# Performance work log

Measured on AMD Instinct MI355X. Metric: run time of the kernel, lower is better.

The kernel has to match this reference:

```python
import jax, jax.numpy as jnp
import numpy as np

B, S, H, V, T = 32, 128, 256, 32000, 100


def setup_inputs() -> dict:
    key = jax.random.key(0)
    ks = jax.random.split(key, 16)
    s = 1.0 / np.sqrt(H)

    def u(k, shape):
        return jax.random.uniform(k, shape, jnp.float32, -s, s)

    return dict(
        enc_outputs=jax.random.normal(ks[0], (B, S, H), jnp.float32),
        enc_hidden=jax.random.normal(ks[1], (1, B, H), jnp.float32),
        target_tensor=jax.random.randint(ks[2], (B, T), 0, V),
        embedding=u(ks[3], (V, H)),
        Qw=u(ks[4], (H, H)), Qb=u(ks[5], (H,)),
        Kw=u(ks[6], (H, H)), Kb=u(ks[7], (H,)),
        Vw=u(ks[8], (1, H)), Vb=u(ks[9], (1,)),
        W_ih=u(ks[10], (3 * H, 2 * H)), W_hh=u(ks[11], (3 * H, H)),
        b_ih=u(ks[12], (3 * H,)), b_hh=u(ks[13], (3 * H,)),
        out_w=u(ks[14], (V, H)), out_b=u(ks[15], (V,)),
    )


def reference(enc_outputs, enc_hidden, target_tensor, embedding,
              Qw, Qb, Kw, Kb, Vw, Vb, W_ih, W_hh, b_ih, b_hh, out_w, out_b):
    # Teacher-forcing decode: dec_input starts at token 0, then target[:, i].
    Bv, Sv, Hd = enc_outputs.shape
    Tv = target_tensor.shape[1]
    # K(keys) is step-invariant: precompute once (same math as in-loop Linear).
    enc_k = enc_outputs @ Kw.T + Kb  # (B,S,H)
    tokens = jnp.concatenate(
        [jnp.zeros((Bv, 1), target_tensor.dtype), target_tensor[:, :-1]], axis=1)
    tokens_t = tokens.T  # (T,B)

    def step(h, tok):
        emb = embedding[tok]                                  # (B,H), dropout=eval noop
        q = h @ Qw.T + Qb                                     # query from hidden
        e = jnp.tanh(q[:, None, :] + enc_k)                   # (B,S,H) additive attn
        scores = jnp.einsum('bsh,h->bs', e, Vw[0]) + Vb[0]    # (B,S)
        w = jax.nn.softmax(scores, axis=-1)
        ctx = jnp.einsum('bs,bsh->bh', w, enc_outputs)        # bmm(weights, keys)
        x = jnp.concatenate([emb, ctx], axis=-1)              # (B,2H)
        gi = x @ W_ih.T + b_ih
        gh = h @ W_hh.T + b_hh
        r = jax.nn.sigmoid(gi[:, :Hd] + gh[:, :Hd])
        z = jax.nn.sigmoid(gi[:, Hd:2 * Hd] + gh[:, Hd:2 * Hd])
        n = jnp.tanh(gi[:, 2 * Hd:] + r * gh[:, 2 * Hd:])
        h_new = (1.0 - z) * n + z * h                         # torch GRU cell
        logits = h_new @ out_w.T + out_b                      # (B,V)
        return h_new, (logits, w)

    h_final, (logits, atts) = jax.lax.scan(step, enc_hidden[0], tokens_t)
    dec_outputs = jax.nn.log_softmax(jnp.transpose(logits, (1, 0, 2)), axis=-1)  # (B,T,V)
    atts = jnp.transpose(atts, (1, 0, 2))                     # (B,T,S)
    return dec_outputs, h_final[None], atts
```

## Files before the change

### kernel.cpp

```cpp
#include <hip/hip_runtime.h>
#include <hip/hip_bf16.h>

#define Bn 32
#define Sn 128
#define Hn 256
#define Vn 32000
#define Tn 100
#define GIn 768
#define AGENT __HIP_MEMORY_SCOPE_AGENT

typedef __attribute__((ext_vector_type(8))) short bf16x8;
typedef __attribute__((ext_vector_type(4))) float f32x4;

__device__ __forceinline__ float frcp(float x){ return __builtin_amdgcn_rcpf(x); }
__device__ __forceinline__ float ftanh(float x){ return 1.0f - 2.0f*frcp(__expf(2.0f*x)+1.0f); }
__device__ __forceinline__ float ftanh_pre(float y){ return 1.0f - 2.0f*frcp(__expf(y)+1.0f); }
__device__ __forceinline__ float fsigm(float x){ return frcp(1.0f + __expf(-x)); }
__device__ __forceinline__ float b2f(unsigned short u){
  unsigned int v = ((unsigned int)u) << 16; return __builtin_bit_cast(float, v);
}
__device__ __forceinline__ unsigned short f2bu(float f){
  unsigned int u = __builtin_bit_cast(unsigned int, f);
  u += 0x7FFFu + ((u >> 16) & 1u);
  return (unsigned short)(u >> 16);
}
__device__ __forceinline__ void st_ag_u(unsigned int* p, unsigned int v){
  __hip_atomic_store(p, v, __ATOMIC_RELAXED, AGENT);
}
__device__ __forceinline__ unsigned int ld_ag_u(unsigned int* p){
  return __hip_atomic_load(p, __ATOMIC_RELAXED, AGENT);
}

__global__ __launch_bounds__(256) void k_tr(const float* __restrict__ in,
    float* __restrict__ out, int R, int C)
{
  __shared__ float tile[32][33];
  const int bx = blockIdx.x*32, by = blockIdx.y*32;
  const int tx = threadIdx.x & 31, ty = threadIdx.x >> 5;
  #pragma unroll
  for(int r = ty; r < 32; r += 8)
    if(by + r < R && bx + tx < C) tile[r][tx] = in[(size_t)(by + r)*C + bx + tx];
  __syncthreads();
  #pragma unroll
  for(int r = ty; r < 32; r += 8)
    if(bx + r < C && by + tx < R) out[(size_t)(bx + r)*R + by + tx] = tile[tx][r];
}

__global__ __launch_bounds__(256) void k_packW1R(const float* __restrict__ Qw,
    const float* __restrict__ Whh, unsigned short* __restrict__ W1R)
{
  const int tid = blockIdx.x*256 + threadIdx.x;
  const int lane = tid & 63;
  const int fragid = tid >> 6;
  const int tt = fragid % 5;
  const int kk = (fragid/5) % 8;
  const int w  = (fragid/40) % 8;
  const int hb = fragid/320;
  const int lr = lane & 15, lg = lane >> 4;
  const float* src;
  if(tt < 2){
    const int f = w*32 + tt*16 + lr;
    src = Qw + (size_t)f*Hn;
  } else {
    const int lf = w*48 + (tt-2)*16 + lr;
    const int g = lf >> 7, jj = lf & 127;
    src = Whh + (size_t)(g*256 + hb*128 + jj)*Hn;
  }
  const int col = kk*32 + lg*8;
  float4 v0 = *(const float4*)(src + col), v1 = *(const float4*)(src + col + 4);
  unsigned short* d = W1R + ((size_t)fragid*64 + lane)*8;
  d[0]=f2bu(v0.x); d[1]=f2bu(v0.y); d[2]=f2bu(v0.z); d[3]=f2bu(v0.w);
  d[4]=f2bu(v1.x); d[5]=f2bu(v1.y); d[6]=f2bu(v1.z); d[7]=f2bu(v1.w);
}

__global__ __launch_bounds__(256) void k_cvt(const float* __restrict__ src,
    __hip_bfloat16* __restrict__ dst, int n)
{
  int i = (blockIdx.x*256 + threadIdx.x)*4;
  if(i < n){
    float4 v = *(const float4*)(src + i);
    dst[i+0] = __float2bfloat16(v.x);
    dst[i+1] = __float2bfloat16(v.y);
    dst[i+2] = __float2bfloat16(v.z);
    dst[i+3] = __float2bfloat16(v.w);
  }
}

__global__ __launch_bounds__(256) void k_enc2(const float* __restrict__ enc_outputs,
    const float* __restrict__ KwT, const float* __restrict__ Kb,
    unsigned short* __restrict__ enc_kb16)
{
  const int r0 = blockIdx.x*16, j = threadIdx.x;
  __shared__ __align__(16) float encl[Hn][20];
  #pragma unroll
  for(int r = 0; r < 16; r++) encl[j][r] = enc_outputs[(size_t)(r0 + r)*Hn + j];
  __syncthreads();
  float acc[16];
  #pragma unroll
  for(int r = 0; r < 16; r++) acc[r] = Kb[j];
  for(int d = 0; d < Hn; d++){
    const float wv = KwT[(size_t)d*Hn + j];
    const float4 e0 = *(const float4*)&encl[d][0];
    const float4 e1 = *(const float4*)&encl[d][4];
    const float4 e2 = *(const float4*)&encl[d][8];
    const float4 e3 = *(const float4*)&encl[d][12];
    acc[0]+=e0.x*wv; acc[1]+=e0.y*wv; acc[2]+=e0.z*wv; acc[3]+=e0.w*wv;
    acc[4]+=e1.x*wv; acc[5]+=e1.y*wv; acc[6]+=e1.z*wv; acc[7]+=e1.w*wv;
    acc[8]+=e2.x*wv; acc[9]+=e2.y*wv; acc[10]+=e2.z*wv; acc[11]+=e2.w*wv;
    acc[12]+=e3.x*wv; acc[13]+=e3.y*wv; acc[14]+=e3.z*wv; acc[15]+=e3.w*wv;
  }
  #pragma unroll
  for(int r = 0; r < 16; r++) enc_kb16[(size_t)(r0 + r)*Hn + j] = f2bu(2.0f*acc[r]);
}

__global__ __launch_bounds__(256) void k_packEk(const unsigned short* __restrict__ enc_kb16,
    unsigned short* __restrict__ ekP)
{
  const int tid = blockIdx.x*256 + threadIdx.x;
  const int b = tid >> 12;
  const int o = tid & 4095;
  const int g = o >> 6, l = o & 63;
  const int w = g >> 3, i = g & 7;
  const int s = w*16 + (l >> 2);
  const int e0 = i*32 + (l & 3)*8;
  const int4 v = *(const int4*)(enc_kb16 + ((size_t)(b*Sn + s))*Hn + e0);
  *(int4*)(ekP + (size_t)b*32768 + (size_t)o*8) = v;
}

__global__ __launch_bounds__(768) void k_encW2F(const float* __restrict__ enc_outputs,
    const float* __restrict__ W_ihT, unsigned short* __restrict__ encW2F)
{
  const int r0 = blockIdx.x*16, tid = threadIdx.x;
  __shared__ __align__(16) float encl[Hn][20];
  if(tid < Hn){
    #pragma unroll
    for(int r = 0; r < 16; r++) encl[tid][r] = enc_outputs[(size_t)(r0 + r)*Hn + tid];
  }
  __syncthreads();
  float acc[16];
  #pragma unroll
  for(int r = 0; r < 16; r++) acc[r] = 0.f;
  for(int d = 0; d < Hn; d++){
    const float wv = W_ihT[(size_t)(Hn + d)*GIn + tid];
    const float4 e0 = *(const float4*)&encl[d][0];
    const float4 e1 = *(const float4*)&encl[d][4];
    const float4 e2 = *(const float4*)&encl[d][8];
    const float4 e3 = *(const float4*)&encl[d][12];
    acc[0]+=e0.x*wv; acc[1]+=e0.y*wv; acc[2]+=e0.z*wv; acc[3]+=e0.w*wv;
    acc[4]+=e1.x*wv; acc[5]+=e1.y*wv; acc[6]+=e1.z*wv; acc[7]+=e1.w*wv;
    acc[8]+=e2.x*wv; acc[9]+=e2.y*wv; acc[10]+=e2.z*wv; acc[11]+=e2.w*wv;
    acc[12]+=e3.x*wv; acc[13]+=e3.y*wv; acc[14]+=e3.z*wv; acc[15]+=e3.w*wv;
  }
  const int g = tid >> 8, jj = tid & 255;
  const int hb = jj >> 7, jl = jj & 127;
  const int c = g*128 + jl;
  const int wvv = c/48, rem = c - wvv*48, tt = rem >> 4, lr = rem & 15;
  #pragma unroll
  for(int r = 0; r < 16; r++){
    const int bs = r0 + r;
    const int bb = bs >> 7, s = bs & 127;
    const int kk = s >> 5, lg = (s >> 3) & 3, e = s & 7;
    const int lane = lg*16 + lr;
    encW2F[(size_t)(bb*2 + hb)*49152 + (size_t)((wvv*12 + tt*4 + kk)*64 + lane)*8 + e]
        = f2bu(acc[r]);
  }
}

__global__ __launch_bounds__(768) void k_giemb2(const int* __restrict__ target,
    const float* __restrict__ embedding, const float* __restrict__ W_ihT,
    const float* __restrict__ b_ih, float* __restrict__ gi_emb)
{
  const int r0 = blockIdx.x*16, tid = threadIdx.x;
  __shared__ __align__(16) float embl[Hn][20];
  if(tid < Hn){
    #pragma unroll
    for(int r = 0; r < 16; r++){
      const int row = r0 + r;
      const int t = row >> 5, b = row & 31;
      const int tok = (t == 0) ? 0 : target[b*Tn + (t-1)];
      embl[tid][r] = embedding[(size_t)tok*Hn + tid];
    }
  }
  __syncthreads();
  float acc[16];
  #pragma unroll
  for(int r = 0; r < 16; r++) acc[r] = b_ih[tid];
  for(int d = 0; d < Hn; d++){
    const float wv = W_ihT[(size_t)d*GIn + tid];
    const float4 e0 = *(const float4*)&embl[d][0];
    const float4 e1 = *(const float4*)&embl[d][4];
    const float4 e2 = *(const float4*)&embl[d][8];
    const float4 e3 = *(const float4*)&embl[d][12];
    acc[0]+=e0.x*wv; acc[1]+=e0.y*wv; acc[2]+=e0.z*wv; acc[3]+=e0.w*wv;
    acc[4]+=e1.x*wv; acc[5]+=e1.y*wv; acc[6]+=e1.z*wv; acc[7]+=e1.w*wv;
    acc[8]+=e2.x*wv; acc[9]+=e2.y*wv; acc[10]+=e2.z*wv; acc[11]+=e2.w*wv;
    acc[12]+=e3.x*wv; acc[13]+=e3.y*wv; acc[14]+=e3.z*wv; acc[15]+=e3.w*wv;
  }
  #pragma unroll
  for(int r = 0; r < 16; r++) gi_emb[(size_t)(r0 + r)*GIn + tid] = acc[r];
}

__global__ __launch_bounds__(512, 2) void k_loop7(
    const float* __restrict__ enc_hidden,
    const unsigned short* __restrict__ ekP,
    const unsigned short* __restrict__ encW2F,
    const unsigned short* __restrict__ W1R,
    const float* __restrict__ Qb, const float* __restrict__ b_hh,
    const float* __restrict__ Vw, const float* __restrict__ Vb,
    const float* __restrict__ gi_emb,
    __hip_bfloat16* __restrict__ h_all,
    float* __restrict__ atts_out,
    float* __restrict__ hfin_out,
    unsigned int* hbuf,
    unsigned int* hflag)
{
  const int bid = blockIdx.x;
  const int hb = (bid >> 3) & 1;
  const int p  = (bid & 7) | ((bid >> 4) << 3);
  const int b = p;
  const int tid = threadIdx.x;
  const int lane = tid & 63, wv = tid >> 6;
  const int lr = lane & 15, lg = lane >> 4;

  __shared__ __align__(16) unsigned short ew_l[49152];
  __shared__ __align__(16) float h_sh[128];
  __shared__ __align__(16) short h_b16[Hn];
  __shared__ __align__(16) float qgh_sh[1024];
  __shared__ __align__(16) float vw_sh[Hn];
  __shared__ __align__(16) float sc_sh[Sn];
  __shared__ __align__(16) unsigned short wb_l[Sn];
  __shared__ __align__(16) float gic_l[384];

  {
    const unsigned short* src = encW2F + (size_t)(b*2 + hb)*49152;
    #pragma unroll
    for(int c = 0; c < 12; c++){
      const int idx = (c*512 + tid)*8;
      *(int4*)(ew_l + idx) = *(const int4*)(src + idx);
    }
  }
  bf16x8 ekr[8];
  {
    const unsigned short* esrc = ekP + (size_t)b*32768;
    #pragma unroll
    for(int i = 0; i < 8; i++)
      ekr[i] = *(const bf16x8*)(esrc + (size_t)((wv*8 + i)*64 + lane)*8);
  }
  bf16x8 w1f[40];
  {
    const unsigned short* wsrc = W1R + (((size_t)(hb*8 + wv)*40)*64 + lane)*8;
    #pragma unroll
    for(int f = 0; f < 40; f++) w1f[f] = *(const bf16x8*)(wsrc + (size_t)f*512);
  }
  float bias_r[5]; int idx_r[5];
  #pragma unroll
  for(int tt = 0; tt < 2; tt++){
    const int f = wv*32 + tt*16 + lr;
    bias_r[tt] = Qb[f]; idx_r[tt] = f;
  }
  #pragma unroll
  for(int tt = 2; tt < 5; tt++){
    const int lf = wv*48 + (tt-2)*16 + lr;
    const int g = lf >> 7, jj = lf & 127;
    bias_r[tt] = b_hh[g*256 + hb*128 + jj];
    idx_r[tt]  = 256 + g*256 + hb*128 + jj;
  }
  if(tid < Hn){
    vw_sh[tid] = Vw[tid];
    h_b16[tid] = (short)f2bu(enc_hidden[b*Hn + tid]);
  }
  if(tid < 128) h_sh[tid] = enc_hidden[b*Hn + hb*128 + tid];
  __syncthreads();
  const float vb0 = Vb[0];
  const int g2 = tid & 3;

  for(int t = 0; t < Tn; t++){
    const int par = t & 1;
    {
      f32x4 acc[5];
      #pragma unroll
      for(int tt = 0; tt < 5; tt++) acc[tt] = (f32x4){0.f,0.f,0.f,0.f};
      #pragma unroll
      for(int kk = 0; kk < 8; kk++){
        bf16x8 a = *(const bf16x8*)(h_b16 + kk*32 + lg*8);
        #pragma unroll
        for(int tt = 0; tt < 5; tt++)
          acc[tt] = __builtin_amdgcn_mfma_f32_16x16x32_bf16(a, w1f[kk*5 + tt], acc[tt], 0, 0, 0);
      }
      if(lane < 16){
        #pragma unroll
        for(int tt = 0; tt < 5; tt++){
          float v = acc[tt][0] + bias_r[tt];
          if(tt < 2) v *= 2.0f;
          qgh_sh[idx_r[tt]] = v;
        }
      }
    }
    __syncthreads();

    {
      float pacc = 0.f;
      #pragma unroll
      for(int i = 0; i < 8; i++){
        const bf16x8 e8 = ekr[i];
        const int kb = i*32 + g2*8;
        #pragma unroll
        for(int j = 0; j < 8; j++){
          float ev = b2f((unsigned short)e8[j]);
          pacc = fmaf(vw_sh[kb + j], ftanh_pre(qgh_sh[kb + j] + ev), pacc);
        }
      }
      pacc += __shfl_xor(pacc, 1); pacc += __shfl_xor(pacc, 2);
      if(g2 == 0) sc_sh[tid >> 2] = pacc + vb0;
    }
    __syncthreads();

    if(tid < 64){
      float v0 = sc_sh[tid], v1 = sc_sh[tid + 64];
      float m = fmaxf(v0, v1);
      #pragma unroll
      for(int off = 1; off < 64; off <<= 1) m = fmaxf(m, __shfl_xor(m, off));
      float e0 = __expf(v0 - m), e1 = __expf(v1 - m);
      float sm = e0 + e1;
      #pragma unroll
      for(int off = 1; off < 64; off <<= 1) sm += __shfl_xor(sm, off);
      float inv = frcp(sm);
      float w0 = e0*inv, w1 = e1*inv;
      wb_l[tid] = f2bu(w0); wb_l[tid + 64] = f2bu(w1);
      if(hb == 0){
        float* ao = atts_out + ((size_t)b*Tn + t)*Sn;
        ao[tid] = w0; ao[tid + 64] = w1;
      }
    }
    float ge0 = 0.f, ge1 = 0.f, ge2 = 0.f;
    if(tid < 128){
      const float* ge = gi_emb + ((size_t)t*Bn + b)*GIn + hb*128 + tid;
      ge0 = ge[0]; ge1 = ge[256]; ge2 = ge[512];
    }
    __syncthreads();

    {
      bf16x8 wfrag[4];
      #pragma unroll
      for(int kk = 0; kk < 4; kk++)
        wfrag[kk] = *(const bf16x8*)(wb_l + kk*32 + lg*8);
      #pragma unroll
      for(int tt = 0; tt < 3; tt++){
        f32x4 a3 = (f32x4){0.f,0.f,0.f,0.f};
        #pragma unroll
        for(int kk = 0; kk < 4; kk++){
          bf16x8 bfr = *(const bf16x8*)(ew_l + (size_t)((wv*12 + tt*4 + kk)*64 + lane)*8);
          a3 = __builtin_amdgcn_mfma_f32_16x16x32_bf16(wfrag[kk], bfr, a3, 0, 0, 0);
        }
        if(lane < 16) gic_l[wv*48 + tt*16 + lane] = a3[0];
      }
    }
    __syncthreads();

    if(tid < 128){
      float gr = ge0 + gic_l[tid];
      float gz = ge1 + gic_l[128 + tid];
      float gn = ge2 + gic_l[256 + tid];
      const int jg = hb*128 + tid;
      float r = fsigm(gr + qgh_sh[256 + jg]);
      float z = fsigm(gz + qgh_sh[512 + jg]);
      float n = ftanh(gn + r*qgh_sh[768 + jg]);
      float hn2 = (1.0f - z)*n + z*h_sh[tid];
      h_sh[tid] = hn2;
      const unsigned short hb16 = f2bu(hn2);
      h_b16[jg] = (short)hb16;
      h_all[((size_t)t*Bn + b)*Hn + jg] = __float2bfloat16(hn2);
      if(t == Tn-1) hfin_out[b*Hn + jg] = hn2;
      if(t < Tn-1){
        float hnx = __shfl_down(hn2, 1);
        if(!(tid & 1)){
          unsigned int u = (unsigned int)hb16 | ((unsigned int)f2bu(hnx) << 16);
          st_ag_u(&hbuf[((size_t)(par*32 + p)*2 + hb)*64 + (tid >> 1)], u);
        }
      }
    }
    __syncthreads();

    if(t < Tn-1){
      if(tid == 0)
        __hip_atomic_store(&hflag[p*2 + hb], (unsigned)(t + 1), __ATOMIC_RELEASE, AGENT);
      if(tid < 64){
        long cnt = 0;
        while(__hip_atomic_load(&hflag[p*2 + (hb^1)], __ATOMIC_ACQUIRE, AGENT) < (unsigned)(t + 1)
              && ++cnt < 10000000L){}
        unsigned int u = ld_ag_u(&hbuf[((size_t)(par*32 + p)*2 + (hb^1))*64 + tid]);
        ((unsigned int*)h_b16)[(hb^1)*64 + tid] = u;
      }
      __syncthreads();
    }
  }
}

__global__ __launch_bounds__(256, 2) void k_lg3(
    const unsigned short* __restrict__ h_all, const unsigned short* __restrict__ w_bf,
    const float* __restrict__ out_b,
    float* __restrict__ pmax, float* __restrict__ psum,
    const float* __restrict__ lse, float* __restrict__ dec_out,
    int pass)
{
  const int tid = threadIdx.x;
  const int lane = tid & 63, w = tid >> 6;
  const int lr = lane & 15, lg = lane >> 4;
  const int wm = w >> 1, wn = w & 1;
  const int m0 = blockIdx.x*128;
  const int n0 = blockIdx.y*128;
  const int nchunk = blockIdx.y;
  __shared__ __align__(16) unsigned short As[2][128][72];
  __shared__ __align__(16) unsigned short Bs[2][128][72];
  const int srow = tid >> 2, scol = (tid & 3)*16;

  f32x4 acc[4][4];
  #pragma unroll
  for(int mt = 0; mt < 4; mt++)
    #pragma unroll
    for(int nt = 0; nt < 4; nt++) acc[mt][nt] = (f32x4){0.f,0.f,0.f,0.f};

  auto stage = [&](int buf, int ks){
    #pragma unroll
    for(int i = 0; i < 2; i++){
      const int r = i*64 + srow;
      const size_t ga = (size_t)(m0 + r)*Hn + ks*64 + scol;
      const size_t gb = (size_t)(n0 + r)*Hn + ks*64 + scol;
      int4 a0 = *(const int4*)(h_all + ga);
      int4 a1 = *(const int4*)(h_all + ga + 8);
      int4 b0 = *(const int4*)(w_bf + gb);
      int4 b1 = *(const int4*)(w_bf + gb + 8);
      *(int4*)(&As[buf][r][scol])     = a0;
      *(int4*)(&As[buf][r][scol + 8]) = a1;
      *(int4*)(&Bs[buf][r][scol])     = b0;
      *(int4*)(&Bs[buf][r][scol + 8]) = b1;
    }
  };
  auto compute = [&](int buf){
    bf16x8 am[4][2], bn[4][2];
    #pragma unroll
    for(int mt = 0; mt < 4; mt++)
      #pragma unroll
      for(int kk = 0; kk < 2; kk++)
        am[mt][kk] = *(const bf16x8*)(&As[buf][wm*64 + mt*16 + lr][kk*32 + lg*8]);
    #pragma unroll
    for(int nt = 0; nt < 4; nt++)
      #pragma unroll
      for(int kk = 0; kk < 2; kk++)
        bn[nt][kk] = *(const bf16x8*)(&Bs[buf][wn*64 + nt*16 + lr][kk*32 + lg*8]);
    #pragma unroll
    for(int kk = 0; kk < 2; kk++)
      #pragma unroll
      for(int mt = 0; mt < 4; mt++)
        #pragma unroll
        for(int nt = 0; nt < 4; nt++)
          acc[mt][nt] = __builtin_amdgcn_mfma_f32_16x16x32_bf16(am[mt][kk], bn[nt][kk], acc[mt][nt], 0, 0, 0);
  };

  stage(0, 0);
  __syncthreads();
  #pragma unroll
  for(int ks = 0; ks < 4; ks++){
    const int buf = ks & 1;
    if(ks < 3) stage(buf^1, ks+1);
    compute(buf);
    __syncthreads();
  }

  float bias[4];
  #pragma unroll
  for(int nt = 0; nt < 4; nt++) bias[nt] = out_b[n0 + wn*64 + nt*16 + lr];

  if(pass == 0){
    __shared__ float pm_l[128][2];
    __shared__ float ps_l[128][2];
    #pragma unroll
    for(int mt = 0; mt < 4; mt++){
      #pragma unroll
      for(int i = 0; i < 4; i++){
        float v0 = acc[mt][0][i] + bias[0], v1 = acc[mt][1][i] + bias[1];
        float v2 = acc[mt][2][i] + bias[2], v3 = acc[mt][3][i] + bias[3];
        float m = fmaxf(fmaxf(v0, v1), fmaxf(v2, v3));
        m = fmaxf(m, __shfl_xor(m, 1)); m = fmaxf(m, __shfl_xor(m, 2));
        m = fmaxf(m, __shfl_xor(m, 4)); m = fmaxf(m, __shfl_xor(m, 8));
        float s = __expf(v0 - m) + __expf(v1 - m) + __expf(v2 - m) + __expf(v3 - m);
        s += __shfl_xor(s, 1); s += __shfl_xor(s, 2);
        s += __shfl_xor(s, 4); s += __shfl_xor(s, 8);
        if(lr == 0){
          const int rl = wm*64 + mt*16 + lg*4 + i;
          pm_l[rl][wn] = m; ps_l[rl][wn] = s;
        }
      }
    }
    __syncthreads();
    if(tid < 128){
      float m = fmaxf(pm_l[tid][0], pm_l[tid][1]);
      float s = ps_l[tid][0]*__expf(pm_l[tid][0] - m) + ps_l[tid][1]*__expf(pm_l[tid][1] - m);
      pmax[(size_t)nchunk*3200 + m0 + tid] = m;
      psum[(size_t)nchunk*3200 + m0 + tid] = s;
    }
  } else {
    #pragma unroll
    for(int mt = 0; mt < 4; mt++){
      #pragma unroll
      for(int i = 0; i < 4; i++){
        const int rg = m0 + wm*64 + mt*16 + lg*4 + i;
        const float l = lse[rg];
        const int bb = rg & 31, tt2 = rg >> 5;
        float* dst = dec_out + (size_t)bb*((size_t)Tn*Vn) + (size_t)tt2*Vn + n0 + wn*64;
        dst[ 0 + lr] = acc[mt][0][i] + bias[0] - l;
        dst[16 + lr] = acc[mt][1][i] + bias[1] - l;
        dst[32 + lr] = acc[mt][2][i] + bias[2] - l;
        dst[48 + lr] = acc[mt][3][i] + bias[3] - l;
      }
    }
  }
}

__global__ __launch_bounds__(256) void k_lse2(const float* __restrict__ pmax,
    const float* __restrict__ psum, float* __restrict__ lse)
{
  const int row = blockIdx.x*64 + (threadIdx.x >> 2);
  const int q = threadIdx.x & 3;
  float m = -3.0e38f;
  for(int c = q; c < 250; c += 4) m = fmaxf(m, pmax[(size_t)c*3200 + row]);
  float mg = m;
  mg = fmaxf(mg, __shfl_xor(mg, 1));
  mg = fmaxf(mg, __shfl_xor(mg, 2));
  float s = 0.f;
  for(int c = q; c < 250; c += 4)
    s += psum[(size_t)c*3200 + row] * __expf(pmax[(size_t)c*3200 + row] - mg);
  s += __shfl_xor(s, 1);
  s += __shfl_xor(s, 2);
  if(q == 0) lse[row] = mg + __logf(s);
}

extern "C" void kernel_launch(void* const* d_in, const int* in_sizes, int n_in,
                              void* d_out, int out_size, void* d_ws, size_t ws_size,
                              hipStream_t stream)
{
  const float* enc_outputs = (const float*)d_in[0];
  const float* enc_hidden  = (const float*)d_in[1];
  const int*   target      = (const int*)d_in[2];
  const float* embedding   = (const float*)d_in[3];
  const float* Qw   = (const float*)d_in[4];
  const float* Qb   = (const float*)d_in[5];
  const float* Kw   = (const float*)d_in[6];
  const float* Kb   = (const float*)d_in[7];
  const float* Vw   = (const float*)d_in[8];
  const float* Vb   = (const float*)d_in[9];
  const float* W_ih = (const float*)d_in[10];
  const float* W_hh = (const float*)d_in[11];
  const float* b_ih = (const float*)d_in[12];
  const float* b_hh = (const float*)d_in[13];
  const float* out_w = (const float*)d_in[14];
  const float* out_b = (const float*)d_in[15];

  float* dec  = (float*)d_out;
  float* hfin = dec + (size_t)Bn*Tn*Vn;
  float* atts = hfin + Bn*Hn;

  unsigned short* enc_kb16 = (unsigned short*)(dec);
  unsigned short* ekP      = (unsigned short*)(dec + 524288);
  unsigned short* encW2F   = (unsigned short*)(dec + 1048576);
  float* gi_emb = dec + 2621440;
  float* W_ihT  = dec + 5079040;
  float* KwT    = dec + 5472256;
  float* pmax   = dec + 5537792;
  float* psum   = dec + 6337792;
  unsigned short* W1R = (unsigned short*)(dec + 7137792);
  unsigned int* hbuf  = (unsigned int*)(dec + 7301632);
  unsigned int* hflag = (unsigned int*)(dec + 7309824);

  float* wsf = (float*)d_ws;
  float* lse = wsf;
  __hip_bfloat16* h_all = (__hip_bfloat16*)(wsf + 3200);
  __hip_bfloat16* w_bf  = h_all + (size_t)Tn*Bn*Hn;

  k_tr     <<<dim3(8, 8),   dim3(256), 0, stream>>>(Kw, KwT, 256, 256);
  k_tr     <<<dim3(16, 24), dim3(256), 0, stream>>>(W_ih, W_ihT, 768, 512);
  k_packW1R<<<dim3(160),    dim3(256), 0, stream>>>(Qw, W_hh, W1R);
  k_cvt    <<<dim3((Vn*Hn)/1024), dim3(256), 0, stream>>>(out_w, w_bf, Vn*Hn);
  k_enc2   <<<dim3(256), dim3(256), 0, stream>>>(enc_outputs, KwT, Kb, enc_kb16);
  k_packEk <<<dim3(512), dim3(256), 0, stream>>>(enc_kb16, ekP);
  k_encW2F <<<dim3(256), dim3(768), 0, stream>>>(enc_outputs, W_ihT, encW2F);
  k_giemb2 <<<dim3(200), dim3(768), 0, stream>>>(target, embedding, W_ihT, b_ih, gi_emb);

  hipMemsetAsync((void*)hflag, 0, 64*sizeof(unsigned int), stream);

  k_loop7 <<<dim3(64), dim3(512), 0, stream>>>(enc_hidden, ekP, encW2F, W1R,
            Qb, b_hh, Vw, Vb, gi_emb, h_all, atts, hfin, hbuf, hflag);

  k_lg3   <<<dim3(25, 250), dim3(256), 0, stream>>>(
            (const unsigned short*)h_all, (const unsigned short*)w_bf, out_b,
            pmax, psum, (const float*)nullptr, (float*)nullptr, 0);
  k_lse2  <<<dim3(50), dim3(256), 0, stream>>>(pmax, psum, lse);
  k_lg3   <<<dim3(25, 250), dim3(256), 0, stream>>>(
            (const unsigned short*)h_all, (const unsigned short*)w_bf, out_b,
            (float*)nullptr, (float*)nullptr, lse, dec, 1);
}
```

Baseline: 1.210 ms.

## Overlap hidden-state exchange with local GEMV half and restage logits GEMM tiles

```diff
diff --git a/kernel.cpp b/kernel.cpp
--- a/kernel.cpp
+++ b/kernel.cpp
@@ -200,7 +200,7 @@
   for(int r = 0; r < 16; r++) gi_emb[(size_t)(r0 + r)*GIn + tid] = acc[r];
 }
 
-__global__ __launch_bounds__(512, 2) void k_loop7(
+__global__ __launch_bounds__(512, 2) void k_loop9(
     const float* __restrict__ enc_hidden,
     const unsigned short* __restrict__ ekP,
     const unsigned short* __restrict__ encW2F,
@@ -275,25 +275,39 @@
   const int g2 = tid & 3;
 
   for(int t = 0; t < Tn; t++){
-    const int par = t & 1;
-    {
-      f32x4 acc[5];
-      #pragma unroll
-      for(int tt = 0; tt < 5; tt++) acc[tt] = (f32x4){0.f,0.f,0.f,0.f};
-      #pragma unroll
-      for(int kk = 0; kk < 8; kk++){
-        bf16x8 a = *(const bf16x8*)(h_b16 + kk*32 + lg*8);
-        #pragma unroll
-        for(int tt = 0; tt < 5; tt++)
-          acc[tt] = __builtin_amdgcn_mfma_f32_16x16x32_bf16(a, w1f[kk*5 + tt], acc[tt], 0, 0, 0);
-      }
-      if(lane < 16){
-        #pragma unroll
-        for(int tt = 0; tt < 5; tt++){
-          float v = acc[tt][0] + bias_r[tt];
-          if(tt < 2) v *= 2.0f;
-          qgh_sh[idx_r[tt]] = v;
-        }
+    f32x4 acc[5];
+    #pragma unroll
+    for(int tt = 0; tt < 5; tt++) acc[tt] = (f32x4){0.f,0.f,0.f,0.f};
+    #pragma unroll
+    for(int kkl = 0; kkl < 4; kkl++){
+      const int kch = hb*4 + kkl;
+      bf16x8 a = *(const bf16x8*)(h_b16 + kch*32 + lg*8);
+      #pragma unroll
+      for(int tt = 0; tt < 5; tt++)
+        acc[tt] = __builtin_amdgcn_mfma_f32_16x16x32_bf16(a, w1f[kch*5 + tt], acc[tt], 0, 0, 0);
+    }
+    if(t > 0 && tid < 64){
+      long cnt = 0;
+      while(__hip_atomic_load(&hflag[p*2 + (hb^1)], __ATOMIC_ACQUIRE, AGENT) < (unsigned)t
+            && ++cnt < 10000000L){}
+      unsigned int u = ld_ag_u(&hbuf[((size_t)((t & 1)*32 + p)*2 + (hb^1))*64 + tid]);
+      ((unsigned int*)h_b16)[(hb^1)*64 + tid] = u;
+    }
+    __syncthreads();
+    #pragma unroll
+    for(int kkl = 0; kkl < 4; kkl++){
+      const int kch = (1 - hb)*4 + kkl;
+      bf16x8 a = *(const bf16x8*)(h_b16 + kch*32 + lg*8);
+      #pragma unroll
+      for(int tt = 0; tt < 5; tt++)
+        acc[tt] = __builtin_amdgcn_mfma_f32_16x16x32_bf16(a, w1f[kch*5 + tt], acc[tt], 0, 0, 0);
+    }
+    if(lane < 16){
+      #pragma unroll
+      for(int tt = 0; tt < 5; tt++){
+        float v = acc[tt][0] + bias_r[tt];
+        if(tt < 2) v *= 2.0f;
+        qgh_sh[idx_r[tt]] = v;
       }
     }
     __syncthreads();
@@ -375,28 +389,17 @@
         float hnx = __shfl_down(hn2, 1);
         if(!(tid & 1)){
           unsigned int u = (unsigned int)hb16 | ((unsigned int)f2bu(hnx) << 16);
-          st_ag_u(&hbuf[((size_t)(par*32 + p)*2 + hb)*64 + (tid >> 1)], u);
+          st_ag_u(&hbuf[((size_t)(((t+1) & 1)*32 + p)*2 + hb)*64 + (tid >> 1)], u);
         }
       }
     }
     __syncthreads();
-
-    if(t < Tn-1){
-      if(tid == 0)
-        __hip_atomic_store(&hflag[p*2 + hb], (unsigned)(t + 1), __ATOMIC_RELEASE, AGENT);
-      if(tid < 64){
-        long cnt = 0;
-        while(__hip_atomic_load(&hflag[p*2 + (hb^1)], __ATOMIC_ACQUIRE, AGENT) < (unsigned)(t + 1)
-              && ++cnt < 10000000L){}
-        unsigned int u = ld_ag_u(&hbuf[((size_t)(par*32 + p)*2 + (hb^1))*64 + tid]);
-        ((unsigned int*)h_b16)[(hb^1)*64 + tid] = u;
-      }
-      __syncthreads();
-    }
-  }
-}
-
-__global__ __launch_bounds__(256, 2) void k_lg3(
+    if(tid == 0 && t < Tn-1)
+      __hip_atomic_store(&hflag[p*2 + hb], (unsigned)(t + 1), __ATOMIC_RELEASE, AGENT);
+  }
+}
+
+__global__ __launch_bounds__(256, 2) void k_lg4(
     const unsigned short* __restrict__ h_all, const unsigned short* __restrict__ w_bf,
     const float* __restrict__ out_b,
     float* __restrict__ pmax, float* __restrict__ psum,
@@ -410,9 +413,27 @@
   const int m0 = blockIdx.x*128;
   const int n0 = blockIdx.y*128;
   const int nchunk = blockIdx.y;
-  __shared__ __align__(16) unsigned short As[2][128][72];
-  __shared__ __align__(16) unsigned short Bs[2][128][72];
-  const int srow = tid >> 2, scol = (tid & 3)*16;
+  __shared__ __align__(16) unsigned short Bs[128*256];
+
+  bf16x8 am[4][8];
+  {
+    const unsigned short* abase = h_all + (size_t)(m0 + wm*64 + lr)*Hn + lg*8;
+    #pragma unroll
+    for(int mt = 0; mt < 4; mt++)
+      #pragma unroll
+      for(int kk = 0; kk < 8; kk++)
+        am[mt][kk] = *(const bf16x8*)(abase + (size_t)(mt*16)*Hn + kk*32);
+  }
+  {
+    #pragma unroll
+    for(int it = 0; it < 16; it++){
+      const int id = it*256 + tid;
+      const int r = id >> 5, c8 = id & 31;
+      const int4 v = *(const int4*)(w_bf + (size_t)(n0 + r)*Hn + c8*8);
+      *(int4*)(Bs + r*256 + ((c8 ^ (r & 7)) << 3)) = v;
+    }
+  }
+  __syncthreads();
 
   f32x4 acc[4][4];
   #pragma unroll
@@ -420,51 +441,20 @@
     #pragma unroll
     for(int nt = 0; nt < 4; nt++) acc[mt][nt] = (f32x4){0.f,0.f,0.f,0.f};
 
-  auto stage = [&](int buf, int ks){
-    #pragma unroll
-    for(int i = 0; i < 2; i++){
-      const int r = i*64 + srow;
-      const size_t ga = (size_t)(m0 + r)*Hn + ks*64 + scol;
-      const size_t gb = (size_t)(n0 + r)*Hn + ks*64 + scol;
-      int4 a0 = *(const int4*)(h_all + ga);
-      int4 a1 = *(const int4*)(h_all + ga + 8);
-      int4 b0 = *(const int4*)(w_bf + gb);
-      int4 b1 = *(const int4*)(w_bf + gb + 8);
-      *(int4*)(&As[buf][r][scol])     = a0;
-      *(int4*)(&As[buf][r][scol + 8]) = a1;
-      *(int4*)(&Bs[buf][r][scol])     = b0;
-      *(int4*)(&Bs[buf][r][scol + 8]) = b1;
-    }
-  };
-  auto compute = [&](int buf){
-    bf16x8 am[4][2], bn[4][2];
+  #pragma unroll
+  for(int kk = 0; kk < 8; kk++){
+    bf16x8 bn[4];
+    #pragma unroll
+    for(int nt = 0; nt < 4; nt++){
+      const int row = wn*64 + nt*16 + lr;
+      const int c8 = kk*4 + lg;
+      bn[nt] = *(const bf16x8*)(Bs + row*256 + ((c8 ^ (row & 7)) << 3));
+    }
     #pragma unroll
     for(int mt = 0; mt < 4; mt++)
       #pragma unroll
-      for(int kk = 0; kk < 2; kk++)
-        am[mt][kk] = *(const bf16x8*)(&As[buf][wm*64 + mt*16 + lr][kk*32 + lg*8]);
-    #pragma unroll
-    for(int nt = 0; nt < 4; nt++)
-      #pragma unroll
-      for(int kk = 0; kk < 2; kk++)
-        bn[nt][kk] = *(const bf16x8*)(&Bs[buf][wn*64 + nt*16 + lr][kk*32 + lg*8]);
-    #pragma unroll
-    for(int kk = 0; kk < 2; kk++)
-      #pragma unroll
-      for(int mt = 0; mt < 4; mt++)
-        #pragma unroll
-        for(int nt = 0; nt < 4; nt++)
-          acc[mt][nt] = __builtin_amdgcn_mfma_f32_16x16x32_bf16(am[mt][kk], bn[nt][kk], acc[mt][nt], 0, 0, 0);
-  };
-
-  stage(0, 0);
-  __syncthreads();
-  #pragma unroll
-  for(int ks = 0; ks < 4; ks++){
-    const int buf = ks & 1;
-    if(ks < 3) stage(buf^1, ks+1);
-    compute(buf);
-    __syncthreads();
+      for(int nt = 0; nt < 4; nt++)
+        acc[mt][nt] = __builtin_amdgcn_mfma_f32_16x16x32_bf16(am[mt][kk], bn[nt], acc[mt][nt], 0, 0, 0);
   }
 
   float bias[4];
@@ -588,14 +578,14 @@
 
   hipMemsetAsync((void*)hflag, 0, 64*sizeof(unsigned int), stream);
 
-  k_loop7 <<<dim3(64), dim3(512), 0, stream>>>(enc_hidden, ekP, encW2F, W1R,
+  k_loop9 <<<dim3(64), dim3(512), 0, stream>>>(enc_hidden, ekP, encW2F, W1R,
             Qb, b_hh, Vw, Vb, gi_emb, h_all, atts, hfin, hbuf, hflag);
 
-  k_lg3   <<<dim3(25, 250), dim3(256), 0, stream>>>(
+  k_lg4   <<<dim3(25, 250), dim3(256), 0, stream>>>(
             (const unsigned short*)h_all, (const unsigned short*)w_bf, out_b,
             pmax, psum, (const float*)nullptr, (float*)nullptr, 0);
   k_lse2  <<<dim3(50), dim3(256), 0, stream>>>(pmax, psum, lse);
-  k_lg3   <<<dim3(25, 250), dim3(256), 0, stream>>>(
+  k_lg4   <<<dim3(25, 250), dim3(256), 0, stream>>>(
             (const unsigned short*)h_all, (const unsigned short*)w_bf, out_b,
             (float*)nullptr, (float*)nullptr, lse, dec, 1);
 }
```

New measurement: 1.792 ms. +48.2%, slower.
